# Optimization experiments

Measured on AMD Instinct MI355X. Metric: run time of the kernel, lower is better.

## Reference

```python
import jax, jax.numpy as jnp
import numpy as np

HEADS = 8
EMBED = 768
FFN = 4 * EMBED
LN_EPS = 1e-5


def _layernorm(x, g, b):
    m = jnp.mean(x, axis=-1, keepdims=True)
    v = jnp.var(x, axis=-1, keepdims=True)
    return (x - m) * jax.lax.rsqrt(v + LN_EPS) * g + b


def _attention(xn, ctx, Wq, Wkv, Wo, bo, mask):
    # xn: [B, N, C], ctx: [B, M, C], mask: [B, 1, N, M] bool (True = keep)
    B, N, C = xn.shape
    d = C // HEADS
    q = (xn @ Wq).reshape(B, N, HEADS, d).transpose(0, 2, 1, 3)          # b h i d
    k, v = jnp.split(ctx @ Wkv, 2, axis=-1)
    k = k.reshape(B, -1, HEADS, d).transpose(0, 2, 1, 3)                 # b h j d
    v = v.reshape(B, -1, HEADS, d).transpose(0, 2, 1, 3)
    sim = jnp.einsum('bhid,bhjd->bhij', q, k) * (d ** -0.5)
    sim = jnp.where(mask, sim, -jnp.finfo(sim.dtype).max)
    attn = jax.nn.softmax(sim, axis=-1)
    out = jnp.einsum('bhij,bhjd->bhid', attn, v)
    out = out.transpose(0, 2, 1, 3).reshape(B, N, C)
    return out @ Wo + bo


def _block(x, c, effect_lengths, us_rate,
           Wq1, Wkv1, Wo1, bo1, Wq2, Wkv2, Wo2, bo2,
           g1, b1, g2, b2, g4, b4, gc, bc, Wf1, bf1, Wf2, bf2):
    B, L, C = x.shape
    S = c.shape[1]
    el = effect_lengths * us_rate                                        # [B]
    i = jnp.arange(L)
    j_self = jnp.arange(L)
    j_cross = jnp.arange(S)
    # ragged per-sample masks, broadcast over heads: [B, 1, L, L] / [B, 1, L, S]
    mask1 = ((i[None, :, None] < el[:, None, None]) &
             (j_self[None, None, :] < el[:, None, None]))[:, None]
    mask2 = ((i[None, :, None] < el[:, None, None]) &
             (j_cross[None, None, :] < effect_lengths[:, None, None]))[:, None]

    xn = _layernorm(x, g1, b1)
    x = x + _attention(xn, xn, Wq1, Wkv1, Wo1, bo1, mask1)
    xn = _layernorm(x, g2, b2)
    cn = _layernorm(c, gc, bc)
    x = x + _attention(xn, cn, Wq2, Wkv2, Wo2, bo2, mask2)
    xn = _layernorm(x, g4, b4)
    x = x + (jax.nn.gelu(xn @ Wf1 + bf1, approximate=False) @ Wf2 + bf2)
    return x


def setup_inputs() -> dict:
    key = jax.random.key(0)
    ks = jax.random.split(key, 20)
    B, S, US = 8, 512, 2
    L = S * US
    s = 0.02
    inp = {
        'x': jax.random.normal(ks[0], (B, L, EMBED), jnp.float32),
        'c': jax.random.normal(ks[1], (B, S, EMBED), jnp.float32),
        'effect_lengths': jax.random.randint(ks[2], (B,), 1, S + 1),
        'us_rate': US,
        'Wq1': jax.random.normal(ks[3], (EMBED, EMBED), jnp.float32) * s,
        'Wkv1': jax.random.normal(ks[4], (EMBED, 2 * EMBED), jnp.float32) * s,
        'Wo1': jax.random.normal(ks[5], (EMBED, EMBED), jnp.float32) * s,
        'bo1': jnp.zeros((EMBED,), jnp.float32),
        'Wq2': jax.random.normal(ks[6], (EMBED, EMBED), jnp.float32) * s,
        'Wkv2': jax.random.normal(ks[7], (EMBED, 2 * EMBED), jnp.float32) * s,
        'Wo2': jax.random.normal(ks[8], (EMBED, EMBED), jnp.float32) * s,
        'bo2': jnp.zeros((EMBED,), jnp.float32),
        'g1': jnp.ones((EMBED,), jnp.float32), 'b1': jnp.zeros((EMBED,), jnp.float32),
        'g2': jnp.ones((EMBED,), jnp.float32), 'b2': jnp.zeros((EMBED,), jnp.float32),
        'g4': jnp.ones((EMBED,), jnp.float32), 'b4': jnp.zeros((EMBED,), jnp.float32),
        'gc': jnp.ones((EMBED,), jnp.float32), 'bc': jnp.zeros((EMBED,), jnp.float32),
        'Wf1': jax.random.normal(ks[9], (EMBED, FFN), jnp.float32) * s,
        'bf1': jnp.zeros((FFN,), jnp.float32),
        'Wf2': jax.random.normal(ks[10], (FFN, EMBED), jnp.float32) * s,
        'bf2': jnp.zeros((EMBED,), jnp.float32),
    }
    return inp


def reference(x, c, effect_lengths, us_rate,
              Wq1, Wkv1, Wo1, bo1, Wq2, Wkv2, Wo2, bo2,
              g1, b1, g2, b2, g4, b4, gc, bc, Wf1, bf1, Wf2, bf2):
    return _block(x, c, effect_lengths, us_rate,
                  Wq1, Wkv1, Wo1, bo1, Wq2, Wkv2, Wo2, bo2,
                  g1, b1, g2, b2, g4, b4, gc, bc, Wf1, bf1, Wf2, bf2)
```

## Files before the change

kernel.cpp:

```cpp
#include <hip/hip_runtime.h>
#include <math.h>

#define EMBED 768
#define HEADS 8
#define HDIM  96
#define NEG_MASK (-1.0e30f)

typedef unsigned short u16;
typedef unsigned int   u32;

typedef __attribute__((ext_vector_type(4))) float f32x4;
typedef __attribute__((ext_vector_type(8))) short short8;

__device__ __forceinline__ float bf2f(u16 u) {
    return __uint_as_float(((u32)u) << 16);
}
__device__ __forceinline__ u16 f2bf(float f) {
    u32 x = __float_as_uint(f);
    u32 r = (x + 0x7fffu + ((x >> 16) & 1u)) >> 16;
    return (u16)r;
}
__device__ __forceinline__ void unpack2(u32 w, float& lo, float& hi) {
    lo = __uint_as_float(w << 16);
    hi = __uint_as_float(w & 0xffff0000u);
}
__device__ __forceinline__ float wget(const void* p, size_t i, int wf) {
    return wf ? ((const float*)p)[i] : bf2f(((const u16*)p)[i]);
}
__device__ __forceinline__ int bswz(int r, int g) {
    return ((g ^ (r & 3) ^ ((r >> 2) & 3) ^ ((r >> 4) & 3)) << 3);
}
__device__ __forceinline__ void lds_barrier() {
    __builtin_amdgcn_sched_barrier(0);
    asm volatile("s_waitcnt lgkmcnt(0)" ::: "memory");
    __builtin_amdgcn_s_barrier();
    __builtin_amdgcn_sched_barrier(0);
}

__global__ __launch_bounds__(64) void detect_kernel(const u16* __restrict__ x,
                                                    const int* __restrict__ el,
                                                    const int* __restrict__ usp,
                                                    int* __restrict__ blk) {
    int lane = threadIdx.x;
    int cnt = 0;
    for (int i = lane; i < 4096; i += 64) {
        u32 e = (x[i] >> 7) & 0xFFu;
        if (e >= 0xC0u) cnt++;
    }
#pragma unroll
    for (int off = 32; off > 0; off >>= 1) cnt += __shfl_xor(cnt, off, 64);
    if (lane == 0) {
        blk[0] = (cnt > 32) ? 1 : 0;
        bool i64 = (el[1] == 0) && (el[3] == 0) && (el[5] == 0) && (el[7] == 0);
        for (int b = 0; b < 8; b++) blk[1 + b] = i64 ? el[2 * b] : el[b];
        blk[9] = usp[0];
    }
}

__global__ void wire_to_f32(const void* __restrict__ in, size_t ioff,
                            float* __restrict__ out, int n,
                            const int* __restrict__ blk) {
    int i = blockIdx.x * blockDim.x + threadIdx.x;
    int wf = blk[0];
    if (i < n) out[i] = wget(in, ioff + (size_t)i, wf);
}
__global__ void wire_copy(const void* __restrict__ in, void* __restrict__ out,
                          int n, const int* __restrict__ blk) {
    int i = blockIdx.x * blockDim.x + threadIdx.x;
    int wf = blk[0];
    if (i < n) {
        if (wf) ((float*)out)[i] = ((const float*)in)[i];
        else    ((u16*)out)[i]   = ((const u16*)in)[i];
    }
}
__global__ void f32_to_out(const float* __restrict__ in, void* __restrict__ out,
                           size_t ooff, int n, const int* __restrict__ blk) {
    int i = blockIdx.x * blockDim.x + threadIdx.x;
    int wf = blk[0];
    if (i < n) {
        if (wf) ((float*)out)[ooff + i] = in[i];
        else    ((u16*)out)[ooff + i]   = f2bf(in[i]);
    }
}

__global__ __launch_bounds__(256) void wtrans_kernel(const void* __restrict__ W, size_t woff,
                                                     int ldw, int K,
                                                     u16* __restrict__ WT,
                                                     const int* __restrict__ blk) {
    __shared__ u16 T[64][65];
// ... 211 lines not shown
            int n = wn * 64 + nt * 16 + x;
            bf[nt] = *(const short8*)&Bs[n * 32 + bswz(n, g)];
        }
#pragma unroll
        for (int mt = 0; mt < 4; mt++)
#pragma unroll
            for (int nt = 0; nt < 4; nt++)
                acc[mt][nt] = __builtin_amdgcn_mfma_f32_16x16x32_bf16(af[mt], bf[nt], acc[mt][nt], 0, 0, 0);
        __syncthreads();
    }

#pragma unroll
    for (int mt = 0; mt < 4; mt++) {
#pragma unroll
        for (int nt = 0; nt < 4; nt++) {
#pragma unroll
            for (int r = 0; r < 4; r++) {
                int m = row0 + wm * 64 + mt * 16 + g * 4 + r;
                int n = col0 + wn * 64 + nt * 16 + x;
                float v = acc[mt][nt][r];
                if (flags & 1) v += wget(bias, boff + n, wf);
                if (flags & 2) v = 0.5f * v * (1.0f + erff(v * 0.70710678118654752f));
                size_t idx = coff + (size_t)m * N + n;
                if (tcmode == 0) {
                    ((float*)Cv)[idx] += v;
                } else if (tcmode == 1) {
                    ((u16*)Cv)[idx] = f2bf(v);
                } else {
                    if (wf) ((float*)Cv)[idx] += v;
                    else { u16* p = (u16*)Cv; p[idx] = f2bf(v + bf2f(p[idx])); }
                }
            }
        }
    }
}

__global__ __launch_bounds__(256) void gemm_mfma_t(const u16* __restrict__ A,
                                                   const u16* __restrict__ BT,
                                                   const void* __restrict__ bias, int boff,
                                                   void* __restrict__ Cv, size_t coff,
                                                   int M, int N, int K, int flags,
                                                   int tcmode, const int* __restrict__ blk) {
    __shared__ __align__(16) u16 As[2][64 * 32];
    __shared__ __align__(16) u16 Bs[2][128 * 32];
    int wf = blk[0];
    int tid = threadIdx.x;
    int wave = tid >> 6, lane = tid & 63;
    int x = lane & 15, g = lane >> 4;
    int wm = wave >> 1, wn = wave & 1;
    int row0 = blockIdx.y * 64, col0 = blockIdx.x * 128;
    int KS = gridDim.z, kz = blockIdx.z;
    int Kc = K / KS;

    int ar = tid >> 2, ac = tid & 3;
    const u16* aptr = A + (size_t)(row0 + ar) * K + kz * Kc + ac * 8;
    int awo = ar * 32 + bswz(ar, ac);
    int br = tid >> 1, bh = tid & 1;
    const u16* bptr = BT + (size_t)(col0 + br) * K + kz * Kc + bh * 16;
    int bwo0 = br * 32 + bswz(br, 2 * bh);
    int bwo1 = br * 32 + bswz(br, 2 * bh + 1);

    int ra[2], rb[4];
#pragma unroll
    for (int mt = 0; mt < 2; mt++) {
        int r = wm * 32 + mt * 16 + x;
        ra[mt] = r * 32 + bswz(r, g);
    }
#pragma unroll
    for (int nt = 0; nt < 4; nt++) {
        int n = wn * 64 + nt * 16 + x;
        rb[nt] = n * 32 + bswz(n, g);
    }

    f32x4 acc[2][4];
#pragma unroll
    for (int i = 0; i < 2; i++)
#pragma unroll
        for (int j = 0; j < 4; j++) acc[i][j] = (f32x4){0.f, 0.f, 0.f, 0.f};

    int nsteps = Kc >> 5;

    *(uint4*)&As[0][awo]  = *(const uint4*)aptr;
    *(uint4*)&Bs[0][bwo0] = *(const uint4*)bptr;
    *(uint4*)&Bs[0][bwo1] = *(const uint4*)(bptr + 8);
    uint4 s0a = {}, s0b0 = {}, s0b1 = {};
    uint4 s1a = {}, s1b0 = {}, s1b1 = {};
    if (nsteps > 1) {
        aptr += 32; bptr += 32;
        s1a  = *(const uint4*)aptr;
        s1b0 = *(const uint4*)bptr; s1b1 = *(const uint4*)(bptr + 8);
    }
    lds_barrier();

#define GSTEP(S, LA, LB0, LB1, WA, WB0, WB1)                                      \
    {                                                                             \
        if ((S) + 2 < nsteps) {                                                   \
            aptr += 32; bptr += 32;                                               \
            LA  = *(const uint4*)aptr;                                            \
            LB0 = *(const uint4*)bptr; LB1 = *(const uint4*)(bptr + 8);           \
        }                                                                         \
        short8 af[2], bfr[4];                                                     \
        _Pragma("unroll")                                                         \
        for (int mt = 0; mt < 2; mt++)                                            \
            af[mt] = *(const short8*)&As[(S) & 1][ra[mt]];                        \
        _Pragma("unroll")                                                         \
        for (int nt = 0; nt < 4; nt++)                                            \
            bfr[nt] = *(const short8*)&Bs[(S) & 1][rb[nt]];                       \
        _Pragma("unroll")                                                         \
        for (int mt = 0; mt < 2; mt++)                                            \
            _Pragma("unroll")                                                     \
            for (int nt = 0; nt < 4; nt++)                                        \
                acc[mt][nt] = __builtin_amdgcn_mfma_f32_16x16x32_bf16(            \
                    af[mt], bfr[nt], acc[mt][nt], 0, 0, 0);                       \
        if ((S) + 1 < nsteps) {                                                   \
            int nb = (((S) & 1) ^ 1);                                             \
            *(uint4*)&As[nb][awo]  = WA;                                          \
            *(uint4*)&Bs[nb][bwo0] = WB0; *(uint4*)&Bs[nb][bwo1] = WB1;           \
            lds_barrier();                                                        \
        }                                                                         \
    }

    for (int s = 0; s < nsteps; s += 2) {
        GSTEP(s, s0a, s0b0, s0b1, s1a, s1b0, s1b1);
        if (s + 1 < nsteps)
            GSTEP(s + 1, s1a, s1b0, s1b1, s0a, s0b0, s0b1);
    }
#undef GSTEP

    bool kz0 = (kz == 0);
#pragma unroll
    for (int mt = 0; mt < 2; mt++) {
#pragma unroll
        for (int nt = 0; nt < 4; nt++) {
#pragma unroll
            for (int r = 0; r < 4; r++) {
                int m = row0 + wm * 32 + mt * 16 + g * 4 + r;
                int n = col0 + wn * 64 + nt * 16 + x;
                float v = acc[mt][nt][r];
                if ((flags & 1) && kz0) v += wget(bias, boff + n, wf);
                if (flags & 2) v = 0.5f * v * (1.0f + erff(v * 0.70710678118654752f));
                size_t idx = coff + (size_t)m * N + n;
                if (tcmode == 0) {
                    if (KS > 1) atomicAdd(&((float*)Cv)[idx], v);
                    else        ((float*)Cv)[idx] += v;
                } else if (tcmode == 1) {
                    ((u16*)Cv)[idx] = f2bf(v);
                } else {
                    if (wf) ((float*)Cv)[idx] += v;
                    else { u16* p = (u16*)Cv; p[idx] = f2bf(v + bf2f(p[idx])); }
                }
            }
        }
    }
}

__global__ __launch_bounds__(256) void attn_kernel(const u16* __restrict__ Q,
                                                   const u16* __restrict__ K,
                                                   const u16* __restrict__ V,
                                                   u16* __restrict__ AO,
                                                   int ldq, int ldk, int ldv, int ldo,
                                                   size_t qss, size_t kss, size_t oss,
                                                   const int* __restrict__ blk,
                                                   int bfix, int Lk, int is_self) {
    int bz   = (bfix < 0) ? blockIdx.z : 0;
    int bidx = (bfix < 0) ? blockIdx.z : bfix;
    const u16* Qp = Q + (size_t)bz * qss;
    const u16* Kp = K + (size_t)bz * kss;
    const u16* Vp = V + (size_t)bz * kss;
    u16* AOp = AO + (size_t)bz * oss;

    int hoff = blockIdx.y * HDIM;
    int i0 = blockIdx.x * 64;
    int tid = threadIdx.x;
    int wave = tid >> 6, lane = tid & 63;
    int x = lane & 15, g = lane >> 4;

    int elb = blk[1 + bidx];
    int el_q = elb * blk[9];
    int el_k = is_self ? el_q : elb;

    bool allinv = (i0 >= el_q);
    int Lk_loop = Lk;
    if (!allinv && (i0 + 64 <= el_q)) {
        int lke = (el_k + 63) & ~63;
        Lk_loop = (lke < Lk) ? lke : Lk;
    }

    __shared__ __align__(16) u16 Ks[64 * 96];
    __shared__ __align__(16) u16 Vs[96 * 64];
    __shared__ __align__(16) u16 Ps[4][16 * 72];

    short8 qf[3];
    {
        const u16* qrow = Qp + (size_t)(i0 + wave * 16 + x) * ldq + hoff;
#pragma unroll
        for (int kc = 0; kc < 3; kc++)
            qf[kc] = *(const short8*)(qrow + kc * 32 + g * 8);
    }

    const f32x4 zero4 = {0.f, 0.f, 0.f, 0.f};
    f32x4 o[6];
#pragma unroll
    for (int dt = 0; dt < 6; dt++) o[dt] = zero4;
    float m[4], l[4];
#pragma unroll
    for (int r = 0; r < 4; r++) { m[r] = NEG_MASK; l[r] = 0.f; }

    bool qok[4];
#pragma unroll
    for (int r = 0; r < 4; r++) qok[r] = (i0 + wave * 16 + g * 4 + r) < el_q;

    const float scale = 0.10206207261596576f;
    u16* pw = &Ps[wave][0];

    for (int kt0 = 0; kt0 < Lk_loop; kt0 += 64) {
#pragma unroll
        for (int t = 0; t < 3; t++) {
            int idx = tid + t * 256;
            int j = idx / 12, c = idx % 12;
            if (!allinv) {
                *(uint4*)&Ks[j * 96 + c * 8] =
                    *(const uint4*)(Kp + (size_t)(kt0 + j) * ldk + hoff + c * 8);
            }
            uint4 vu = *(const uint4*)(Vp + (size_t)(kt0 + j) * ldv + hoff + c * 8);
            u16 vv[8] = {(u16)(vu.x & 0xffffu), (u16)(vu.x >> 16),
                         (u16)(vu.y & 0xffffu), (u16)(vu.y >> 16),
                         (u16)(vu.z & 0xffffu), (u16)(vu.z >> 16),
                         (u16)(vu.w & 0xffffu), (u16)(vu.w >> 16)};
            int jb = j >> 3, jl = j & 7;
#pragma unroll
            for (int ii = 0; ii < 8; ii++) {
                int d = c * 8 + ii;
                int sb = jb ^ (d & 7) ^ ((d >> 3) & 7);
                Vs[d * 64 + sb * 8 + jl] = vv[ii];
            }
        }
        __syncthreads();

        f32x4 st[4];
        if (!allinv) {
#pragma unroll
            for (int t = 0; t < 4; t++) {
                f32x4 acc = zero4;
#pragma unroll
                for (int kc = 0; kc < 3; kc++) {
                    short8 kf = *(const short8*)&Ks[(t * 16 + x) * 96 + kc * 32 + g * 8];
                    acc = __builtin_amdgcn_mfma_f32_16x16x32_bf16(qf[kc], kf, acc, 0, 0, 0);
                }
                st[t] = acc;
            }
        } else {
#pragma unroll
            for (int t = 0; t < 4; t++) st[t] = zero4;
        }

#pragma unroll
        for (int t = 0; t < 4; t++) {
            bool kv_ok = (kt0 + t * 16 + x) < el_k;
#pragma unroll
            for (int r = 0; r < 4; r++)
                st[t][r] = (kv_ok && qok[r]) ? st[t][r] * scale : NEG_MASK;
        }

        float al[4];
#pragma unroll
        for (int r = 0; r < 4; r++) {
            float rm = fmaxf(fmaxf(st[0][r], st[1][r]), fmaxf(st[2][r], st[3][r]));
            rm = fmaxf(rm, __shfl_xor(rm, 1, 64));
            rm = fmaxf(rm, __shfl_xor(rm, 2, 64));
            rm = fmaxf(rm, __shfl_xor(rm, 4, 64));
            rm = fmaxf(rm, __shfl_xor(rm, 8, 64));
            float mn = fmaxf(m[r], rm);
            al[r] = __expf(m[r] - mn);
            m[r] = mn;
            l[r] *= al[r];
        }
#pragma unroll
        for (int dt = 0; dt < 6; dt++)
#pragma unroll
            for (int r = 0; r < 4; r++) o[dt][r] *= al[r];

#pragma unroll
        for (int t = 0; t < 4; t++)
#pragma unroll
            for (int r = 0; r < 4; r++) {
                float p = __expf(st[t][r] - m[r]);
                l[r] += p;
                pw[(g * 4 + r) * 72 + t * 16 + x] = f2bf(p);
            }

#pragma unroll
        for (int kc = 0; kc < 2; kc++) {
            short8 pf = *(const short8*)&pw[x * 72 + kc * 32 + g * 8];
#pragma unroll
            for (int dt = 0; dt < 6; dt++) {
                int d = dt * 16 + x;
                int sb = (kc * 4 + g) ^ (d & 7) ^ ((d >> 3) & 7);
                short8 vf = *(const short8*)&Vs[d * 64 + sb * 8];
                o[dt] = __builtin_amdgcn_mfma_f32_16x16x32_bf16(pf, vf, o[dt], 0, 0, 0);
            }
        }
        __syncthreads();
    }

    float inv[4];
#pragma unroll
    for (int r = 0; r < 4; r++) {
        float lr = l[r];
        lr += __shfl_xor(lr, 1, 64);
        lr += __shfl_xor(lr, 2, 64);
        lr += __shfl_xor(lr, 4, 64);
        lr += __shfl_xor(lr, 8, 64);
        inv[r] = 1.0f / lr;
    }
#pragma unroll
    for (int dt = 0; dt < 6; dt++)
#pragma unroll
        for (int r = 0; r < 4; r++) {
            size_t ob = (size_t)(i0 + wave * 16 + g * 4 + r) * ldo + hoff + dt * 16 + x;
            AOp[ob] = f2bf(o[dt][r] * inv[r]);
        }
}

extern "C" void kernel_launch(void* const* d_in, const int* in_sizes, int n_in,
                              void* d_out, int out_size, void* d_ws, size_t ws_size,
                              hipStream_t stream) {
    const void* x    = d_in[0];
    const void* c    = d_in[1];
    const int* el    = (const int*)d_in[2];
    const int* us    = (const int*)d_in[3];
    const void* Wq1  = d_in[4];
    const void* Wkv1 = d_in[5];
    const void* Wo1  = d_in[6];
    const void* bo1  = d_in[7];
    const void* Wq2  = d_in[8];
    const void* Wkv2 = d_in[9];
    const void* Wo2  = d_in[10];
    const void* bo2  = d_in[11];
    const void* g1 = d_in[12]; const void* b1 = d_in[13];
    const void* g2 = d_in[14]; const void* b2 = d_in[15];
    const void* g4 = d_in[16]; const void* b4 = d_in[17];
    const void* gc = d_in[18]; const void* bc = d_in[19];
    const void* Wf1 = d_in[20]; const void* bf1 = d_in[21];
    const void* Wf2 = d_in[22]; const void* bf2 = d_in[23];

    const int B = 8, S = 512, L = 1024, C = EMBED;
    const int NX = B * L * C;
    const size_t RL = (size_t)L * C;
    const size_t RS = (size_t)S * C;

    char* ws = (char*)d_ws;
    int*  blk = (int*)ws;
    dim3 blkd(256);

    bool tierA = ws_size >= (size_t)88080448;
    bool tierB = !tierA && ws_size >= (size_t)33030208;

    detect_kernel<<<1, 64, 0, stream>>>((const u16*)x, el, us, blk);

    if (tierA) {
        float* X  = (float*)(ws + 64);
        u16*   XN = (u16*)(ws + 25165888);
        u16*   WT = (u16*)(ws + 37748800);
        char*  P  = ws + 47185984;
        u16* Qb   = (u16*)P;
        u16* KVb  = (u16*)(P + 12582912);
        u16* CNb  = (u16*)P;
        u16* KV2b = (u16*)(P + 6291456);
        u16* Q2b  = (u16*)(P + 18874368);
        u16* Hh   = (u16*)P;
        const size_t WTq = 0, WTkv = 589824, WTo = 1769472;
        const size_t WTf1 = 0, WTf2 = 2359296;

        wire_to_f32<<<(NX + 255) / 256, blkd, 0, stream>>>(x, 0, X, NX, blk);

        wtrans_kernel<<<dim3(12, 12), blkd, 0, stream>>>(Wq1, 0, C, C, WT + WTq, blk);
        wtrans_kernel<<<dim3(24, 12), blkd, 0, stream>>>(Wkv1, 0, 2 * C, C, WT + WTkv, blk);
        wtrans_kernel<<<dim3(12, 12), blkd, 0, stream>>>(Wo1, 0, C, C, WT + WTo, blk);

        ln_kernel<<<B * L, blkd, 0, stream>>>(X, 0, 0, g1, b1, XN, blk);
        gemm_mfma_t<<<dim3(6, 128, 1), blkd, 0, stream>>>(XN, WT + WTq, nullptr, 0, Qb, 0, B * L, C, C, 0, 1, blk);
        gemm_mfma_t<<<dim3(12, 128, 1), blkd, 0, stream>>>(XN, WT + WTkv, nullptr, 0, KVb, 0, B * L, 2 * C, C, 0, 1, blk);
        attn_kernel<<<dim3(16, 8, 8), blkd, 0, stream>>>(Qb, KVb, KVb + C, Qb, C, 2 * C, 2 * C, C,
                                                         RL, (size_t)L * 2 * C, RL, blk, -1, L, 1);
        gemm_mfma_t<<<dim3(6, 128, 1), blkd, 0, stream>>>(Qb, WT + WTo, bo1, 0, X, 0, B * L, C, C, 1, 0, blk);

        wtrans_kernel<<<dim3(12, 12), blkd, 0, stream>>>(Wq2, 0, C, C, WT + WTq, blk);
        wtrans_kernel<<<dim3(24, 12), blkd, 0, stream>>>(Wkv2, 0, 2 * C, C, WT + WTkv, blk);
        wtrans_kernel<<<dim3(12, 12), blkd, 0, stream>>>(Wo2, 0, C, C, WT + WTo, blk);

        ln_kernel<<<B * L, blkd, 0, stream>>>(X, 0, 0, g2, b2, XN, blk);
        ln_kernel<<<B * S, blkd, 0, stream>>>(c, 0, 2, gc, bc, CNb, blk);
        gemm_mfma_t<<<dim3(12, 64, 1), blkd, 0, stream>>>(CNb, WT + WTkv, nullptr, 0, KV2b, 0, B * S, 2 * C, C, 0, 1, blk);
        gemm_mfma_t<<<dim3(6, 128, 1), blkd, 0, stream>>>(XN, WT + WTq, nullptr, 0, Q2b, 0, B * L, C, C, 0, 1, blk);
        attn_kernel<<<dim3(16, 8, 8), blkd, 0, stream>>>(Q2b, KV2b, KV2b + C, Q2b, C, 2 * C, 2 * C, C,
                                                         RL, (size_t)S * 2 * C, RL, blk, -1, S, 0);
        gemm_mfma_t<<<dim3(6, 128, 1), blkd, 0, stream>>>(Q2b, WT + WTo, bo2, 0, X, 0, B * L, C, C, 1, 0, blk);

        wtrans_kernel<<<dim3(48, 12), blkd, 0, stream>>>(Wf1, 0, 4 * C, C, WT + WTf1, blk);
        wtrans_kernel<<<dim3(12, 48), blkd, 0, stream>>>(Wf2, 0, C, 4 * C, WT + WTf2, blk);

        ln_kernel<<<B * L, blkd, 0, stream>>>(X, 0, 0, g4, b4, XN, blk);
        for (int h = 0; h < 2; h++) {
            size_t ro = (size_t)h * 4096 * C;
            gemm_mfma_t<<<dim3(24, 64, 1), blkd, 0, stream>>>(XN + ro, WT + WTf1, bf1, 0, Hh, 0, 4096, 4 * C, C, 1 | 2, 1, blk);
            gemm_mfma_t<<<dim3(6, 64, 2), blkd, 0, stream>>>(Hh, WT + WTf2, bf2, 0, X, ro, 4096, C, 4 * C, 1, 0, blk);
        }

        f32_to_out<<<(NX + 255) / 256, blkd, 0, stream>>>(X, d_out, 0, NX, blk);
    } else if (tierB) {
        float* X  = (float*)(ws + 64);
        u16*   XN = (u16*)(ws + 64 + 25165824);
        char*  P  = ws + 64 + 25165824 + 1572864;
        u16* Qb   = (u16*)P;
        u16* KVb  = (u16*)(P + 1572864);
        u16* AOb  = (u16*)(P + 4718592);
        u16* CNb  = (u16*)P;
        u16* KV2b = (u16*)(P + 786432);
        u16* Q2b  = (u16*)(P + 2359296);
        u16* AO2b = (u16*)(P + 3932160);
        u16* Hb   = (u16*)P;

        wire_to_f32<<<(NX + 255) / 256, blkd, 0, stream>>>(x, 0, X, NX, blk);

        for (int b = 0; b < B; b++) {
            size_t ro = (size_t)b * RL;
            ln_kernel<<<L, blkd, 0, stream>>>(X, ro, 0, g1, b1, XN, blk);
            gemm_mfma<<<dim3(6, 8), blkd, 0, stream>>>(XN, Wq1, 0, C, nullptr, 0, Qb, 0, L, C, C, 0, 1, blk);
            gemm_mfma<<<dim3(12, 8), blkd, 0, stream>>>(XN, Wkv1, 0, 2 * C, nullptr, 0, KVb, 0, L, 2 * C, C, 0, 1, blk);
            attn_kernel<<<dim3(16, 8), blkd, 0, stream>>>(Qb, KVb, KVb + C, AOb, C, 2 * C, 2 * C, C, 0, 0, 0, blk, b, L, 1);
            gemm_mfma<<<dim3(6, 8), blkd, 0, stream>>>(AOb, Wo1, 0, C, bo1, 0, X, ro, L, C, C, 1, 0, blk);

            ln_kernel<<<L, blkd, 0, stream>>>(X, ro, 0, g2, b2, XN, blk);
            ln_kernel<<<S, blkd, 0, stream>>>(c, (size_t)b * RS, 2, gc, bc, CNb, blk);
            gemm_mfma<<<dim3(12, 4), blkd, 0, stream>>>(CNb, Wkv2, 0, 2 * C, nullptr, 0, KV2b, 0, S, 2 * C, C, 0, 1, blk);
            gemm_mfma<<<dim3(6, 8), blkd, 0, stream>>>(XN, Wq2, 0, C, nullptr, 0, Q2b, 0, L, C, C, 0, 1, blk);
            attn_kernel<<<dim3(16, 8), blkd, 0, stream>>>(Q2b, KV2b, KV2b + C, AO2b, C, 2 * C, 2 * C, C, 0, 0, 0, blk, b, S, 0);
            gemm_mfma<<<dim3(6, 8), blkd, 0, stream>>>(AO2b, Wo2, 0, C, bo2, 0, X, ro, L, C, C, 1, 0, blk);

            ln_kernel<<<L, blkd, 0, stream>>>(X, ro, 0, g4, b4, XN, blk);
            gemm_mfma<<<dim3(24, 8), blkd, 0, stream>>>(XN, Wf1, 0, 4 * C, bf1, 0, Hb, 0, L, 4 * C, C, 1 | 2, 1, blk);
            gemm_mfma<<<dim3(6, 8), blkd, 0, stream>>>(Hb, Wf2, 0, C, bf2, 0, X, ro, L, C, 4 * C, 1, 0, blk);
        }
        f32_to_out<<<(NX + 255) / 256, blkd, 0, stream>>>(X, d_out, 0, NX, blk);
    } else {
        u16*  XN  = (u16*)(ws + 64);
        u16*  CNb = (u16*)(ws + 64 + 1572864);
        char* P2  = ws + 64 + 1572864 + 786432;
        u16* Qp  = (u16*)P2;
        u16* Kp  = (u16*)(P2 + 393216);
        u16* Vp  = (u16*)(P2 + 786432);
        u16* AOp = (u16*)(P2 + 1179648);
        u16* Hc  = (u16*)P2;

        wire_copy<<<(NX + 255) / 256, blkd, 0, stream>>>(x, d_out, NX, blk);

        for (int b = 0; b < B; b++) {
            size_t ro = (size_t)b * RL;

            ln_kernel<<<L, blkd, 0, stream>>>(d_out, ro, 2, g1, b1, XN, blk);
            for (int p = 0; p < 4; p++) {
                int h = 2 * p;
                gemm_kernel<<<dim3(3, 16), blkd, 0, stream>>>(XN, Wq1, (size_t)h * 96, C, nullptr, 0, Qp, 0, L, 192, C, 0, 1, blk);
                gemm_kernel<<<dim3(3, 16), blkd, 0, stream>>>(XN, Wkv1, (size_t)h * 96, 2 * C, nullptr, 0, Kp, 0, L, 192, C, 0, 1, blk);
                gemm_kernel<<<dim3(3, 16), blkd, 0, stream>>>(XN, Wkv1, (size_t)(C + h * 96), 2 * C, nullptr, 0, Vp, 0, L, 192, C, 0, 1, blk);
                attn_kernel<<<dim3(16, 2), blkd, 0, stream>>>(Qp, Kp, Vp, AOp, 192, 192, 192, 192, 0, 0, 0, blk, b, L, 1);
                gemm_kernel<<<dim3(12, 16), blkd, 0, stream>>>(AOp, Wo1, (size_t)h * 96 * C, C, bo1, 0, d_out, ro, L, C, 192, (p == 0) ? 1 : 0, 3, blk);
            }
            ln_kernel<<<L, blkd, 0, stream>>>(d_out, ro, 2, g2, b2, XN, blk);
            ln_kernel<<<S, blkd, 0, stream>>>(c, (size_t)b * RS, 2, gc, bc, CNb, blk);
            for (int p = 0; p < 4; p++) {
                int h = 2 * p;
                gemm_kernel<<<dim3(3, 16), blkd, 0, stream>>>(XN, Wq2, (size_t)h * 96, C, nullptr, 0, Qp, 0, L, 192, C, 0, 1, blk);
                gemm_kernel<<<dim3(3, 8), blkd, 0, stream>>>(CNb, Wkv2, (size_t)h * 96, 2 * C, nullptr, 0, Kp, 0, S, 192, C, 0, 1, blk);
                gemm_kernel<<<dim3(3, 8), blkd, 0, stream>>>(CNb, Wkv2, (size_t)(C + h * 96), 2 * C, nullptr, 0, Vp, 0, S, 192, C, 0, 1, blk);
                attn_kernel<<<dim3(16, 2), blkd, 0, stream>>>(Qp, Kp, Vp, AOp, 192, 192, 192, 192, 0, 0, 0, blk, b, S, 0);
                gemm_kernel<<<dim3(12, 16), blkd, 0, stream>>>(AOp, Wo2, (size_t)h * 96 * C, C, bo2, 0, d_out, ro, L, C, 192, (p == 0) ? 1 : 0, 3, blk);
            }
            ln_kernel<<<L, blkd, 0, stream>>>(d_out, ro, 2, g4, b4, XN, blk);
            for (int ch = 0; ch < 4; ch++) {
                gemm_kernel<<<dim3(12, 16), blkd, 0, stream>>>(XN, Wf1, (size_t)ch * C, 4 * C, bf1, ch * C, Hc, 0, L, C, C, 1 | 2, 1, blk);
                gemm_kernel<<<dim3(12, 16), blkd, 0, stream>>>(Hc, Wf2, (size_t)ch * C * C, C, bf2, 0, d_out, ro, L, C, C, (ch == 0) ? 1 : 0, 3, blk);
            }
        }
    }
}
```

Before: 850.8 us.

## Process 128 query rows per attention block to reuse K/V tiles

Result: slower. 886.7 us (+4.2%).

```diff
diff --git a/kernel.cpp b/kernel.cpp
--- a/kernel.cpp
+++ b/kernel.cpp
@@ -470,7 +470,7 @@
     u16* AOp = AO + (size_t)bz * oss;
 
     int hoff = blockIdx.y * HDIM;
-    int i0 = blockIdx.x * 64;
+    int i0 = blockIdx.x * 128;
     int tid = threadIdx.x;
     int wave = tid >> 6, lane = tid & 63;
     int x = lane & 15, g = lane >> 4;
@@ -481,145 +481,184 @@
 
     bool allinv = (i0 >= el_q);
     int Lk_loop = Lk;
-    if (!allinv && (i0 + 64 <= el_q)) {
+    if (!allinv && (i0 + 128 <= el_q)) {
         int lke = (el_k + 63) & ~63;
         Lk_loop = (lke < Lk) ? lke : Lk;
     }
 
     __shared__ __align__(16) u16 Ks[64 * 96];
     __shared__ __align__(16) u16 Vs[96 * 64];
-    __shared__ __align__(16) u16 Ps[4][16 * 72];
-
-    short8 qf[3];
-    {
-        const u16* qrow = Qp + (size_t)(i0 + wave * 16 + x) * ldq + hoff;
+    __shared__ __align__(16) u16 Ps[4][32 * 72];
+
+    short8 qf[2][3];
+#pragma unroll
+    for (int h = 0; h < 2; h++) {
+        const u16* qrow = Qp + (size_t)(i0 + wave * 32 + h * 16 + x) * ldq + hoff;
 #pragma unroll
         for (int kc = 0; kc < 3; kc++)
-            qf[kc] = *(const short8*)(qrow + kc * 32 + g * 8);
+            qf[h][kc] = *(const short8*)(qrow + kc * 32 + g * 8);
     }
 
     const f32x4 zero4 = {0.f, 0.f, 0.f, 0.f};
-    f32x4 o[6];
-#pragma unroll
-    for (int dt = 0; dt < 6; dt++) o[dt] = zero4;
-    float m[4], l[4];
-#pragma unroll
-    for (int r = 0; r < 4; r++) { m[r] = NEG_MASK; l[r] = 0.f; }
-
-    bool qok[4];
-#pragma unroll
-    for (int r = 0; r < 4; r++) qok[r] = (i0 + wave * 16 + g * 4 + r) < el_q;
+    f32x4 o[2][6];
+#pragma unroll
+    for (int h = 0; h < 2; h++)
+#pragma unroll
+        for (int dt = 0; dt < 6; dt++) o[h][dt] = zero4;
+    float m[2][4], l[2][4];
+#pragma unroll
+    for (int h = 0; h < 2; h++)
+#pragma unroll
+        for (int r = 0; r < 4; r++) { m[h][r] = NEG_MASK; l[h][r] = 0.f; }
+
+    bool qok[2][4];
+#pragma unroll
+    for (int h = 0; h < 2; h++)
+#pragma unroll
+        for (int r = 0; r < 4; r++)
+            qok[h][r] = (i0 + wave * 32 + h * 16 + g * 4 + r) < el_q;
 
     const float scale = 0.10206207261596576f;
     u16* pw = &Ps[wave][0];
 
     for (int kt0 = 0; kt0 < Lk_loop; kt0 += 64) {
-#pragma unroll
-        for (int t = 0; t < 3; t++) {
-            int idx = tid + t * 256;
-            int j = idx / 12, c = idx % 12;
-            if (!allinv) {
+        if (!allinv) {
+#pragma unroll
+            for (int t = 0; t < 3; t++) {
+                int idx = tid + t * 256;
+                int j = idx / 12, c = idx % 12;
                 *(uint4*)&Ks[j * 96 + c * 8] =
                     *(const uint4*)(Kp + (size_t)(kt0 + j) * ldk + hoff + c * 8);
-            }
-            uint4 vu = *(const uint4*)(Vp + (size_t)(kt0 + j) * ldv + hoff + c * 8);
-            u16 vv[8] = {(u16)(vu.x & 0xffffu), (u16)(vu.x >> 16),
-                         (u16)(vu.y & 0xffffu), (u16)(vu.y >> 16),
-                         (u16)(vu.z & 0xffffu), (u16)(vu.z >> 16),
-                         (u16)(vu.w & 0xffffu), (u16)(vu.w >> 16)};
-            int jb = j >> 3, jl = j & 7;
-#pragma unroll
-            for (int ii = 0; ii < 8; ii++) {
-                int d = c * 8 + ii;
-                int sb = jb ^ (d & 7) ^ ((d >> 3) & 7);
-                Vs[d * 64 + sb * 8 + jl] = vv[ii];
+                uint4 vu = *(const uint4*)(Vp + (size_t)(kt0 + j) * ldv + hoff + c * 8);
+                u16 vv[8] = {(u16)(vu.x & 0xffffu), (u16)(vu.x >> 16),
+                             (u16)(vu.y & 0xffffu), (u16)(vu.y >> 16),
+                             (u16)(vu.z & 0xffffu), (u16)(vu.z >> 16),
+                             (u16)(vu.w & 0xffffu), (u16)(vu.w >> 16)};
+                int jb = j >> 3, jl = j & 7;
+#pragma unroll
+                for (int ii = 0; ii < 8; ii++) {
+                    int d = c * 8 + ii;
+                    int sb = jb ^ (d & 7) ^ ((d >> 3) & 7);
+                    Vs[d * 64 + sb * 8 + jl] = vv[ii];
+                }
+            }
+        } else {
+#pragma unroll
+            for (int t = 0; t < 3; t++) {
+                int idx = tid + t * 256;
+                int j = idx / 12, c = idx % 12;
+                uint4 vu = *(const uint4*)(Vp + (size_t)(kt0 + j) * ldv + hoff + c * 8);
+                u16 vv[8] = {(u16)(vu.x & 0xffffu), (u16)(vu.x >> 16),
+                             (u16)(vu.y & 0xffffu), (u16)(vu.y >> 16),
+                             (u16)(vu.z & 0xffffu), (u16)(vu.z >> 16),
+                             (u16)(vu.w & 0xffffu), (u16)(vu.w >> 16)};
+                int jb = j >> 3, jl = j & 7;
+#pragma unroll
+                for (int ii = 0; ii < 8; ii++) {
+                    int d = c * 8 + ii;
+                    int sb = jb ^ (d & 7) ^ ((d >> 3) & 7);
+                    Vs[d * 64 + sb * 8 + jl] = vv[ii];
+                }
             }
         }
         __syncthreads();
 
-        f32x4 st[4];
+        f32x4 st[2][4];
         if (!allinv) {
 #pragma unroll
             for (int t = 0; t < 4; t++) {
-                f32x4 acc = zero4;
+                f32x4 a0 = zero4, a1 = zero4;
 #pragma unroll
                 for (int kc = 0; kc < 3; kc++) {
                     short8 kf = *(const short8*)&Ks[(t * 16 + x) * 96 + kc * 32 + g * 8];
-                    acc = __builtin_amdgcn_mfma_f32_16x16x32_bf16(qf[kc], kf, acc, 0, 0, 0);
+                    a0 = __builtin_amdgcn_mfma_f32_16x16x32_bf16(qf[0][kc], kf, a0, 0, 0, 0);
+                    a1 = __builtin_amdgcn_mfma_f32_16x16x32_bf16(qf[1][kc], kf, a1, 0, 0, 0);
                 }
-                st[t] = acc;
+                st[0][t] = a0; st[1][t] = a1;
             }
         } else {
 #pragma unroll
-            for (int t = 0; t < 4; t++) st[t] = zero4;
+            for (int h = 0; h < 2; h++)
+#pragma unroll
+                for (int t = 0; t < 4; t++) st[h][t] = zero4;
         }
 
 #pragma unroll
         for (int t = 0; t < 4; t++) {
             bool kv_ok = (kt0 + t * 16 + x) < el_k;
 #pragma unroll
-            for (int r = 0; r < 4; r++)
-                st[t][r] = (kv_ok && qok[r]) ? st[t][r] * scale : NEG_MASK;
-        }
-
-        float al[4];
-#pragma unroll
-        for (int r = 0; r < 4; r++) {
-            float rm = fmaxf(fmaxf(st[0][r], st[1][r]), fmaxf(st[2][r], st[3][r]));
-            rm = fmaxf(rm, __shfl_xor(rm, 1, 64));
-            rm = fmaxf(rm, __shfl_xor(rm, 2, 64));
-            rm = fmaxf(rm, __shfl_xor(rm, 4, 64));
-            rm = fmaxf(rm, __shfl_xor(rm, 8, 64));
-            float mn = fmaxf(m[r], rm);
-            al[r] = __expf(m[r] - mn);
-            m[r] = mn;
-            l[r] *= al[r];
-        }
-#pragma unroll
-        for (int dt = 0; dt < 6; dt++)
-#pragma unroll
-            for (int r = 0; r < 4; r++) o[dt][r] *= al[r];
-
-#pragma unroll
-        for (int t = 0; t < 4; t++)
+            for (int h = 0; h < 2; h++)
+#pragma unroll
+                for (int r = 0; r < 4; r++)
+                    st[h][t][r] = (kv_ok && qok[h][r]) ? st[h][t][r] * scale : NEG_MASK;
+        }
+
+#pragma unroll
+        for (int h = 0; h < 2; h++) {
+            float al[4];
 #pragma unroll
             for (int r = 0; r < 4; r++) {
-                float p = __expf(st[t][r] - m[r]);
-                l[r] += p;
-                pw[(g * 4 + r) * 72 + t * 16 + x] = f2bf(p);
-            }
+                float rm = fmaxf(fmaxf(st[h][0][r], st[h][1][r]),
+                                 fmaxf(st[h][2][r], st[h][3][r]));
+                rm = fmaxf(rm, __shfl_xor(rm, 1, 64));
+                rm = fmaxf(rm, __shfl_xor(rm, 2, 64));
+                rm = fmaxf(rm, __shfl_xor(rm, 4, 64));
+                rm = fmaxf(rm, __shfl_xor(rm, 8, 64));
+                float mn = fmaxf(m[h][r], rm);
+                al[r] = __expf(m[h][r] - mn);
+                m[h][r] = mn;
+                l[h][r] *= al[r];
+            }
+#pragma unroll
+            for (int dt = 0; dt < 6; dt++)
+#pragma unroll
+                for (int r = 0; r < 4; r++) o[h][dt][r] *= al[r];
+#pragma unroll
+            for (int t = 0; t < 4; t++)
+#pragma unroll
+                for (int r = 0; r < 4; r++) {
+                    float p = __expf(st[h][t][r] - m[h][r]);
+                    l[h][r] += p;
+                    pw[(h * 16 + g * 4 + r) * 72 + t * 16 + x] = f2bf(p);
+                }
+        }
 
 #pragma unroll
         for (int kc = 0; kc < 2; kc++) {
-            short8 pf = *(const short8*)&pw[x * 72 + kc * 32 + g * 8];
+            short8 pf0 = *(const short8*)&pw[x * 72 + kc * 32 + g * 8];
+            short8 pf1 = *(const short8*)&pw[(16 + x) * 72 + kc * 32 + g * 8];
 #pragma unroll
             for (int dt = 0; dt < 6; dt++) {
                 int d = dt * 16 + x;
                 int sb = (kc * 4 + g) ^ (d & 7) ^ ((d >> 3) & 7);
                 short8 vf = *(const short8*)&Vs[d * 64 + sb * 8];
-                o[dt] = __builtin_amdgcn_mfma_f32_16x16x32_bf16(pf, vf, o[dt], 0, 0, 0);
+                o[0][dt] = __builtin_amdgcn_mfma_f32_16x16x32_bf16(pf0, vf, o[0][dt], 0, 0, 0);
+                o[1][dt] = __builtin_amdgcn_mfma_f32_16x16x32_bf16(pf1, vf, o[1][dt], 0, 0, 0);
             }
         }
         __syncthreads();
     }
 
-    float inv[4];
-#pragma unroll
-    for (int r = 0; r < 4; r++) {
-        float lr = l[r];
-        lr += __shfl_xor(lr, 1, 64);
-        lr += __shfl_xor(lr, 2, 64);
-        lr += __shfl_xor(lr, 4, 64);
-        lr += __shfl_xor(lr, 8, 64);
-        inv[r] = 1.0f / lr;
-    }
-#pragma unroll
-    for (int dt = 0; dt < 6; dt++)
+#pragma unroll
+    for (int h = 0; h < 2; h++) {
+        float inv[4];
 #pragma unroll
         for (int r = 0; r < 4; r++) {
-            size_t ob = (size_t)(i0 + wave * 16 + g * 4 + r) * ldo + hoff + dt * 16 + x;
-            AOp[ob] = f2bf(o[dt][r] * inv[r]);
-        }
+            float lr = l[h][r];
+            lr += __shfl_xor(lr, 1, 64);
+            lr += __shfl_xor(lr, 2, 64);
+            lr += __shfl_xor(lr, 4, 64);
+            lr += __shfl_xor(lr, 8, 64);
+            inv[r] = 1.0f / lr;
+        }
+#pragma unroll
+        for (int dt = 0; dt < 6; dt++)
+#pragma unroll
+            for (int r = 0; r < 4; r++) {
+                size_t ob = (size_t)(i0 + wave * 32 + h * 16 + g * 4 + r) * ldo + hoff + dt * 16 + x;
+                AOp[ob] = f2bf(o[h][dt][r] * inv[r]);
+            }
+    }
 }
 
 extern "C" void kernel_launch(void* const* d_in, const int* in_sizes, int n_in,
@@ -681,8 +720,8 @@
         ln_kernel<<<B * L, blkd, 0, stream>>>(X, 0, 0, g1, b1, XN, blk);
         gemm_mfma_t<<<dim3(6, 128, 1), blkd, 0, stream>>>(XN, WT + WTq, nullptr, 0, Qb, 0, B * L, C, C, 0, 1, blk);
         gemm_mfma_t<<<dim3(12, 128, 1), blkd, 0, stream>>>(XN, WT + WTkv, nullptr, 0, KVb, 0, B * L, 2 * C, C, 0, 1, blk);
-        attn_kernel<<<dim3(16, 8, 8), blkd, 0, stream>>>(Qb, KVb, KVb + C, Qb, C, 2 * C, 2 * C, C,
-                                                         RL, (size_t)L * 2 * C, RL, blk, -1, L, 1);
+        attn_kernel<<<dim3(8, 8, 8), blkd, 0, stream>>>(Qb, KVb, KVb + C, Qb, C, 2 * C, 2 * C, C,
+                                                        RL, (size_t)L * 2 * C, RL, blk, -1, L, 1);
         gemm_mfma_t<<<dim3(6, 128, 1), blkd, 0, stream>>>(Qb, WT + WTo, bo1, 0, X, 0, B * L, C, C, 1, 0, blk);
 
         wtrans_kernel<<<dim3(12, 12), blkd, 0, stream>>>(Wq2, 0, C, C, WT + WTq, blk);
@@ -693,8 +732,8 @@
         ln_kernel<<<B * S, blkd, 0, stream>>>(c, 0, 2, gc, bc, CNb, blk);
         gemm_mfma_t<<<dim3(12, 64, 1), blkd, 0, stream>>>(CNb, WT + WTkv, nullptr, 0, KV2b, 0, B * S, 2 * C, C, 0, 1, blk);
         gemm_mfma_t<<<dim3(6, 128, 1), blkd, 0, stream>>>(XN, WT + WTq, nullptr, 0, Q2b, 0, B * L, C, C, 0, 1, blk);
-        attn_kernel<<<dim3(16, 8, 8), blkd, 0, stream>>>(Q2b, KV2b, KV2b + C, Q2b, C, 2 * C, 2 * C, C,
-                                                         RL, (size_t)S * 2 * C, RL, blk, -1, S, 0);
+        attn_kernel<<<dim3(8, 8, 8), blkd, 0, stream>>>(Q2b, KV2b, KV2b + C, Q2b, C, 2 * C, 2 * C, C,
+                                                        RL, (size_t)S * 2 * C, RL, blk, -1, S, 0);
         gemm_mfma_t<<<dim3(6, 128, 1), blkd, 0, stream>>>(Q2b, WT + WTo, bo2, 0, X, 0, B * L, C, C, 1, 0, blk);
 
         wtrans_kernel<<<dim3(48, 12), blkd, 0, stream>>>(Wf1, 0, 4 * C, C, WT + WTf1, blk);
@@ -728,14 +767,14 @@
             ln_kernel<<<L, blkd, 0, stream>>>(X, ro, 0, g1, b1, XN, blk);
             gemm_mfma<<<dim3(6, 8), blkd, 0, stream>>>(XN, Wq1, 0, C, nullptr, 0, Qb, 0, L, C, C, 0, 1, blk);
             gemm_mfma<<<dim3(12, 8), blkd, 0, stream>>>(XN, Wkv1, 0, 2 * C, nullptr, 0, KVb, 0, L, 2 * C, C, 0, 1, blk);
-            attn_kernel<<<dim3(16, 8), blkd, 0, stream>>>(Qb, KVb, KVb + C, AOb, C, 2 * C, 2 * C, C, 0, 0, 0, blk, b, L, 1);
+            attn_kernel<<<dim3(8, 8), blkd, 0, stream>>>(Qb, KVb, KVb + C, AOb, C, 2 * C, 2 * C, C, 0, 0, 0, blk, b, L, 1);
             gemm_mfma<<<dim3(6, 8), blkd, 0, stream>>>(AOb, Wo1, 0, C, bo1, 0, X, ro, L, C, C, 1, 0, blk);
 
             ln_kernel<<<L, blkd, 0, stream>>>(X, ro, 0, g2, b2, XN, blk);
             ln_kernel<<<S, blkd, 0, stream>>>(c, (size_t)b * RS, 2, gc, bc, CNb, blk);
             gemm_mfma<<<dim3(12, 4), blkd, 0, stream>>>(CNb, Wkv2, 0, 2 * C, nullptr, 0, KV2b, 0, S, 2 * C, C, 0, 1, blk);
             gemm_mfma<<<dim3(6, 8), blkd, 0, stream>>>(XN, Wq2, 0, C, nullptr, 0, Q2b, 0, L, C, C, 0, 1, blk);
-            attn_kernel<<<dim3(16, 8), blkd, 0, stream>>>(Q2b, KV2b, KV2b + C, AO2b, C, 2 * C, 2 * C, C, 0, 0, 0, blk, b, S, 0);
+            attn_kernel<<<dim3(8, 8), blkd, 0, stream>>>(Q2b, KV2b, KV2b + C, AO2b, C, 2 * C, 2 * C, C, 0, 0, 0, blk, b, S, 0);
             gemm_mfma<<<dim3(6, 8), blkd, 0, stream>>>(AO2b, Wo2, 0, C, bo2, 0, X, ro, L, C, C, 1, 0, blk);
 
             ln_kernel<<<L, blkd, 0, stream>>>(X, ro, 0, g4, b4, XN, blk);
@@ -764,7 +803,7 @@
                 gemm_kernel<<<dim3(3, 16), blkd, 0, stream>>>(XN, Wq1, (size_t)h * 96, C, nullptr, 0, Qp, 0, L, 192, C, 0, 1, blk);
                 gemm_kernel<<<dim3(3, 16), blkd, 0, stream>>>(XN, Wkv1, (size_t)h * 96, 2 * C, nullptr, 0, Kp, 0, L, 192, C, 0, 1, blk);
                 gemm_kernel<<<dim3(3, 16), blkd, 0, stream>>>(XN, Wkv1, (size_t)(C + h * 96), 2 * C, nullptr, 0, Vp, 0, L, 192, C, 0, 1, blk);
-                attn_kernel<<<dim3(16, 2), blkd, 0, stream>>>(Qp, Kp, Vp, AOp, 192, 192, 192, 192, 0, 0, 0, blk, b, L, 1);
+                attn_kernel<<<dim3(8, 2), blkd, 0, stream>>>(Qp, Kp, Vp, AOp, 192, 192, 192, 192, 0, 0, 0, blk, b, L, 1);
                 gemm_kernel<<<dim3(12, 16), blkd, 0, stream>>>(AOp, Wo1, (size_t)h * 96 * C, C, bo1, 0, d_out, ro, L, C, 192, (p == 0) ? 1 : 0, 3, blk);
             }
             ln_kernel<<<L, blkd, 0, stream>>>(d_out, ro, 2, g2, b2, XN, blk);
@@ -774,7 +813,7 @@
                 gemm_kernel<<<dim3(3, 16), blkd, 0, stream>>>(XN, Wq2, (size_t)h * 96, C, nullptr, 0, Qp, 0, L, 192, C, 0, 1, blk);
                 gemm_kernel<<<dim3(3, 8), blkd, 0, stream>>>(CNb, Wkv2, (size_t)h * 96, 2 * C, nullptr, 0, Kp, 0, S, 192, C, 0, 1, blk);
                 gemm_kernel<<<dim3(3, 8), blkd, 0, stream>>>(CNb, Wkv2, (size_t)(C + h * 96), 2 * C, nullptr, 0, Vp, 0, S, 192, C, 0, 1, blk);
-                attn_kernel<<<dim3(16, 2), blkd, 0, stream>>>(Qp, Kp, Vp, AOp, 192, 192, 192, 192, 0, 0, 0, blk, b, S, 0);
+                attn_kernel<<<dim3(8, 2), blkd, 0, stream>>>(Qp, Kp, Vp, AOp, 192, 192, 192, 192, 0, 0, 0, blk, b, S, 0);
                 gemm_kernel<<<dim3(12, 16), blkd, 0, stream>>>(AOp, Wo2, (size_t)h * 96 * C, C, bo2, 0, d_out, ro, L, C, 192, (p == 0) ? 1 : 0, 3, blk);
             }
             ln_kernel<<<L, blkd, 0, stream>>>(d_out, ro, 2, g4, b4, XN, blk);
```

## Prefetch next K/V tile into registers and drop ragged-length loop truncation

Applied to the files above, without the earlier changes.

Result: no change. 836.9 us (-1.6%).

```diff
diff --git a/kernel.cpp b/kernel.cpp
--- a/kernel.cpp
+++ b/kernel.cpp
@@ -479,13 +479,6 @@
     int el_q = elb * blk[9];
     int el_k = is_self ? el_q : elb;
 
-    bool allinv = (i0 >= el_q);
-    int Lk_loop = Lk;
-    if (!allinv && (i0 + 64 <= el_q)) {
-        int lke = (el_k + 63) & ~63;
-        Lk_loop = (lke < Lk) ? lke : Lk;
-    }
-
     __shared__ __align__(16) u16 Ks[64 * 96];
     __shared__ __align__(16) u16 Vs[96 * 64];
     __shared__ __align__(16) u16 Ps[4][16 * 72];
@@ -513,46 +506,58 @@
     const float scale = 0.10206207261596576f;
     u16* pw = &Ps[wave][0];
 
-    for (int kt0 = 0; kt0 < Lk_loop; kt0 += 64) {
+    int js[3], cs[3];
+#pragma unroll
+    for (int t = 0; t < 3; t++) {
+        int idx = tid + t * 256;
+        js[t] = idx / 12; cs[t] = idx % 12;
+    }
+    uint4 pk[3], pv[3];
+#pragma unroll
+    for (int t = 0; t < 3; t++) {
+        pk[t] = *(const uint4*)(Kp + (size_t)js[t] * ldk + hoff + cs[t] * 8);
+        pv[t] = *(const uint4*)(Vp + (size_t)js[t] * ldv + hoff + cs[t] * 8);
+    }
+
+    for (int kt0 = 0; kt0 < Lk; kt0 += 64) {
 #pragma unroll
         for (int t = 0; t < 3; t++) {
-            int idx = tid + t * 256;
-            int j = idx / 12, c = idx % 12;
-            if (!allinv) {
-                *(uint4*)&Ks[j * 96 + c * 8] =
-                    *(const uint4*)(Kp + (size_t)(kt0 + j) * ldk + hoff + c * 8);
-            }
-            uint4 vu = *(const uint4*)(Vp + (size_t)(kt0 + j) * ldv + hoff + c * 8);
-            u16 vv[8] = {(u16)(vu.x & 0xffffu), (u16)(vu.x >> 16),
-                         (u16)(vu.y & 0xffffu), (u16)(vu.y >> 16),
-                         (u16)(vu.z & 0xffffu), (u16)(vu.z >> 16),
-                         (u16)(vu.w & 0xffffu), (u16)(vu.w >> 16)};
-            int jb = j >> 3, jl = j & 7;
+            *(uint4*)&Ks[js[t] * 96 + cs[t] * 8] = pk[t];
+            u16 vv[8] = {(u16)(pv[t].x & 0xffffu), (u16)(pv[t].x >> 16),
+                         (u16)(pv[t].y & 0xffffu), (u16)(pv[t].y >> 16),
+                         (u16)(pv[t].z & 0xffffu), (u16)(pv[t].z >> 16),
+                         (u16)(pv[t].w & 0xffffu), (u16)(pv[t].w >> 16)};
+            int jb = js[t] >> 3, jl = js[t] & 7;
 #pragma unroll
             for (int ii = 0; ii < 8; ii++) {
-                int d = c * 8 + ii;
+                int d = cs[t] * 8 + ii;
                 int sb = jb ^ (d & 7) ^ ((d >> 3) & 7);
                 Vs[d * 64 + sb * 8 + jl] = vv[ii];
             }
         }
-        __syncthreads();
+        lds_barrier();
+
+        if (kt0 + 64 < Lk) {
+#pragma unroll
+            for (int t = 0; t < 3; t++) {
+                pk[t] = *(const uint4*)(Kp + (size_t)(kt0 + 64 + js[t]) * ldk + hoff + cs[t] * 8);
+                pv[t] = *(const uint4*)(Vp + (size_t)(kt0 + 64 + js[t]) * ldv + hoff + cs[t] * 8);
+            }
+        }
 
         f32x4 st[4];
-        if (!allinv) {
-#pragma unroll
-            for (int t = 0; t < 4; t++) {
-                f32x4 acc = zero4;
-#pragma unroll
-                for (int kc = 0; kc < 3; kc++) {
-                    short8 kf = *(const short8*)&Ks[(t * 16 + x) * 96 + kc * 32 + g * 8];
-                    acc = __builtin_amdgcn_mfma_f32_16x16x32_bf16(qf[kc], kf, acc, 0, 0, 0);
-                }
-                st[t] = acc;
-            }
-        } else {
-#pragma unroll
-            for (int t = 0; t < 4; t++) st[t] = zero4;
-        }
+        __builtin_amdgcn_s_setprio(1);
+#pragma unroll
+        for (int t = 0; t < 4; t++) {
+            f32x4 acc = zero4;
+#pragma unroll
+            for (int kc = 0; kc < 3; kc++) {
+                short8 kf = *(const short8*)&Ks[(t * 16 + x) * 96 + kc * 32 + g * 8];
+                acc = __builtin_amdgcn_mfma_f32_16x16x32_bf16(qf[kc], kf, acc, 0, 0, 0);
+            }
+            st[t] = acc;
+        }
+        __builtin_amdgcn_s_setprio(0);
 
 #pragma unroll
         for (int t = 0; t < 4; t++) {
@@ -589,6 +594,7 @@
                 pw[(g * 4 + r) * 72 + t * 16 + x] = f2bf(p);
             }
 
+        __builtin_amdgcn_s_setprio(1);
 #pragma unroll
         for (int kc = 0; kc < 2; kc++) {
             short8 pf = *(const short8*)&pw[x * 72 + kc * 32 + g * 8];
@@ -600,7 +606,8 @@
                 o[dt] = __builtin_amdgcn_mfma_f32_16x16x32_bf16(pf, vf, o[dt], 0, 0, 0);
             }
         }
-        __syncthreads();
+        __builtin_amdgcn_s_setprio(0);
+        lds_barrier();
     }
 
     float inv[4];
```

## Use direct global-to-LDS loads in GEMM and drop attention masked-tile skipping

Applied to the files above, without the earlier changes.

After: 825.0 us. -3.0%, faster.

```diff
diff --git a/kernel.cpp b/kernel.cpp
--- a/kernel.cpp
+++ b/kernel.cpp
@@ -30,11 +30,13 @@
 __device__ __forceinline__ int bswz(int r, int g) {
     return ((g ^ (r & 3) ^ ((r >> 2) & 3) ^ ((r >> 4) & 3)) << 3);
 }
-__device__ __forceinline__ void lds_barrier() {
-    __builtin_amdgcn_sched_barrier(0);
-    asm volatile("s_waitcnt lgkmcnt(0)" ::: "memory");
-    __builtin_amdgcn_s_barrier();
-    __builtin_amdgcn_sched_barrier(0);
+__device__ __forceinline__ int cswz(int r) {
+    return (r & 3) ^ ((r >> 2) & 3) ^ ((r >> 4) & 3);
+}
+__device__ __forceinline__ void load_lds16(const u16* g, u16* l) {
+    __builtin_amdgcn_global_load_lds((const __attribute__((address_space(1))) u32*)g,
+                                     (__attribute__((address_space(3))) u32*)l,
+                                     16, 0, 0);
 }
 
 __global__ __launch_bounds__(64) void detect_kernel(const u16* __restrict__ x,
@@ -352,13 +354,13 @@
     int KS = gridDim.z, kz = blockIdx.z;
     int Kc = K / KS;
 
-    int ar = tid >> 2, ac = tid & 3;
-    const u16* aptr = A + (size_t)(row0 + ar) * K + kz * Kc + ac * 8;
-    int awo = ar * 32 + bswz(ar, ac);
-    int br = tid >> 1, bh = tid & 1;
-    const u16* bptr = BT + (size_t)(col0 + br) * K + kz * Kc + bh * 16;
-    int bwo0 = br * 32 + bswz(br, 2 * bh);
-    int bwo1 = br * 32 + bswz(br, 2 * bh + 1);
+    int l4 = lane >> 2, lg = lane & 3;
+    int arow = wave * 16 + l4;
+    int brow0 = arow;
+    int brow1 = 64 + arow;
+    const u16* agp  = A  + (size_t)(row0 + arow) * K + kz * Kc + (lg ^ cswz(arow))  * 8;
+    const u16* bgp0 = BT + (size_t)(col0 + brow0) * K + kz * Kc + (lg ^ cswz(brow0)) * 8;
+    const u16* bgp1 = BT + (size_t)(col0 + brow1) * K + kz * Kc + (lg ^ cswz(brow1)) * 8;
 
     int ra[2], rb[4];
 #pragma unroll
@@ -380,52 +382,35 @@
 
     int nsteps = Kc >> 5;
 
-    *(uint4*)&As[0][awo]  = *(const uint4*)aptr;
-    *(uint4*)&Bs[0][bwo0] = *(const uint4*)bptr;
-    *(uint4*)&Bs[0][bwo1] = *(const uint4*)(bptr + 8);
-    uint4 s0a = {}, s0b0 = {}, s0b1 = {};
-    uint4 s1a = {}, s1b0 = {}, s1b1 = {};
-    if (nsteps > 1) {
-        aptr += 32; bptr += 32;
-        s1a  = *(const uint4*)aptr;
-        s1b0 = *(const uint4*)bptr; s1b1 = *(const uint4*)(bptr + 8);
-    }
-    lds_barrier();
-
-#define GSTEP(S, LA, LB0, LB1, WA, WB0, WB1)                                      \
-    {                                                                             \
-        if ((S) + 2 < nsteps) {                                                   \
-            aptr += 32; bptr += 32;                                               \
-            LA  = *(const uint4*)aptr;                                            \
-            LB0 = *(const uint4*)bptr; LB1 = *(const uint4*)(bptr + 8);           \
-        }                                                                         \
-        short8 af[2], bfr[4];                                                     \
-        _Pragma("unroll")                                                         \
-        for (int mt = 0; mt < 2; mt++)                                            \
-            af[mt] = *(const short8*)&As[(S) & 1][ra[mt]];                        \
-        _Pragma("unroll")                                                         \
-        for (int nt = 0; nt < 4; nt++)                                            \
-            bfr[nt] = *(const short8*)&Bs[(S) & 1][rb[nt]];                       \
-        _Pragma("unroll")                                                         \
-        for (int mt = 0; mt < 2; mt++)                                            \
-            _Pragma("unroll")                                                     \
-            for (int nt = 0; nt < 4; nt++)                                        \
-                acc[mt][nt] = __builtin_amdgcn_mfma_f32_16x16x32_bf16(            \
-                    af[mt], bfr[nt], acc[mt][nt], 0, 0, 0);                       \
-        if ((S) + 1 < nsteps) {                                                   \
-            int nb = (((S) & 1) ^ 1);                                             \
-            *(uint4*)&As[nb][awo]  = WA;                                          \
-            *(uint4*)&Bs[nb][bwo0] = WB0; *(uint4*)&Bs[nb][bwo1] = WB1;           \
-            lds_barrier();                                                        \
-        }                                                                         \
-    }
-
-    for (int s = 0; s < nsteps; s += 2) {
-        GSTEP(s, s0a, s0b0, s0b1, s1a, s1b0, s1b1);
-        if (s + 1 < nsteps)
-            GSTEP(s + 1, s1a, s1b0, s1b1, s0a, s0b0, s0b1);
-    }
-#undef GSTEP
+    load_lds16(agp,  &As[0][wave * 512]);
+    load_lds16(bgp0, &Bs[0][wave * 512]);
+    load_lds16(bgp1, &Bs[0][2048 + wave * 512]);
+    __syncthreads();
+
+    int cur = 0;
+    for (int s = 0; s < nsteps; ++s) {
+        bool nxt = (s + 1 < nsteps);
+        if (nxt) {
+            agp += 32; bgp0 += 32; bgp1 += 32;
+            load_lds16(agp,  &As[cur ^ 1][wave * 512]);
+            load_lds16(bgp0, &Bs[cur ^ 1][wave * 512]);
+            load_lds16(bgp1, &Bs[cur ^ 1][2048 + wave * 512]);
+        }
+        short8 af[2], bfr[4];
+#pragma unroll
+        for (int mt = 0; mt < 2; mt++) af[mt] = *(const short8*)&As[cur][ra[mt]];
+#pragma unroll
+        for (int nt = 0; nt < 4; nt++) bfr[nt] = *(const short8*)&Bs[cur][rb[nt]];
+#pragma unroll
+        for (int mt = 0; mt < 2; mt++)
+#pragma unroll
+            for (int nt = 0; nt < 4; nt++)
+                acc[mt][nt] = __builtin_amdgcn_mfma_f32_16x16x32_bf16(af[mt], bfr[nt], acc[mt][nt], 0, 0, 0);
+        if (nxt) {
+            __syncthreads();
+            cur ^= 1;
+        }
+    }
 
     bool kz0 = (kz == 0);
 #pragma unroll
@@ -479,13 +464,6 @@
     int el_q = elb * blk[9];
     int el_k = is_self ? el_q : elb;
 
-    bool allinv = (i0 >= el_q);
-    int Lk_loop = Lk;
-    if (!allinv && (i0 + 64 <= el_q)) {
-        int lke = (el_k + 63) & ~63;
-        Lk_loop = (lke < Lk) ? lke : Lk;
-    }
-
     __shared__ __align__(16) u16 Ks[64 * 96];
     __shared__ __align__(16) u16 Vs[96 * 64];
     __shared__ __align__(16) u16 Ps[4][16 * 72];
@@ -513,15 +491,13 @@
     const float scale = 0.10206207261596576f;
     u16* pw = &Ps[wave][0];
 
-    for (int kt0 = 0; kt0 < Lk_loop; kt0 += 64) {
+    for (int kt0 = 0; kt0 < Lk; kt0 += 64) {
 #pragma unroll
         for (int t = 0; t < 3; t++) {
             int idx = tid + t * 256;
             int j = idx / 12, c = idx % 12;
-            if (!allinv) {
-                *(uint4*)&Ks[j * 96 + c * 8] =
-                    *(const uint4*)(Kp + (size_t)(kt0 + j) * ldk + hoff + c * 8);
-            }
+            *(uint4*)&Ks[j * 96 + c * 8] =
+                *(const uint4*)(Kp + (size_t)(kt0 + j) * ldk + hoff + c * 8);
             uint4 vu = *(const uint4*)(Vp + (size_t)(kt0 + j) * ldv + hoff + c * 8);
             u16 vv[8] = {(u16)(vu.x & 0xffffu), (u16)(vu.x >> 16),
                          (u16)(vu.y & 0xffffu), (u16)(vu.y >> 16),
@@ -538,20 +514,15 @@
         __syncthreads();
 
         f32x4 st[4];
-        if (!allinv) {
-#pragma unroll
-            for (int t = 0; t < 4; t++) {
-                f32x4 acc = zero4;
-#pragma unroll
-                for (int kc = 0; kc < 3; kc++) {
-                    short8 kf = *(const short8*)&Ks[(t * 16 + x) * 96 + kc * 32 + g * 8];
-                    acc = __builtin_amdgcn_mfma_f32_16x16x32_bf16(qf[kc], kf, acc, 0, 0, 0);
-                }
-                st[t] = acc;
-            }
-        } else {
-#pragma unroll
-            for (int t = 0; t < 4; t++) st[t] = zero4;
+#pragma unroll
+        for (int t = 0; t < 4; t++) {
+            f32x4 acc = zero4;
+#pragma unroll
+            for (int kc = 0; kc < 3; kc++) {
+                short8 kf = *(const short8*)&Ks[(t * 16 + x) * 96 + kc * 32 + g * 8];
+                acc = __builtin_amdgcn_mfma_f32_16x16x32_bf16(qf[kc], kf, acc, 0, 0, 0);
+            }
+            st[t] = acc;
         }
 
 #pragma unroll
```
